# Kernel optimization log

Measured on AMD Instinct MI355X. Metric: run time of the kernel, lower is better.

The kernel has to match this reference:

```python
import jax, jax.numpy as jnp
import numpy as np

B, S, D = 4, 2048, 1024
H = 16
DH = D // H          # 64
DFF = 4096
EPS = 1e-5


def _layer_norm(x, gamma, beta):
    mu = jnp.mean(x, axis=-1, keepdims=True)
    var = jnp.mean(jnp.square(x - mu), axis=-1, keepdims=True)
    return (x - mu) * jax.lax.rsqrt(var + EPS) * gamma + beta


def setup_inputs() -> dict:
    key = jax.random.key(0)
    ks = jax.random.split(key, 8)
    s_in = 1.0 / np.sqrt(D)
    s_ff = 1.0 / np.sqrt(DFF)
    return {
        "x": jax.random.normal(ks[0], (B, S, D), dtype=jnp.float32),
        # per-head qkv weights stacked: [H, D, 3*DH] (nn.Linear, bias=False)
        "Wqkv": jax.random.normal(ks[1], (H, D, 3 * DH), dtype=jnp.float32) * s_in,
        "Wproj": jax.random.normal(ks[2], (D, D), dtype=jnp.float32) * s_in,
        "bproj": jnp.zeros((D,), dtype=jnp.float32),
        "ln1_g": jnp.ones((D,), dtype=jnp.float32),
        "ln1_b": jnp.zeros((D,), dtype=jnp.float32),
        "ln2_g": jnp.ones((D,), dtype=jnp.float32),
        "ln2_b": jnp.zeros((D,), dtype=jnp.float32),
        "W1": jax.random.normal(ks[3], (D, DFF), dtype=jnp.float32) * s_in,
        "b1": jnp.zeros((DFF,), dtype=jnp.float32),
        "W2": jax.random.normal(ks[4], (DFF, D), dtype=jnp.float32) * s_ff,
        "b2": jnp.zeros((D,), dtype=jnp.float32),
    }


def reference(x, Wqkv, Wproj, bproj, ln1_g, ln1_b, ln2_g, ln2_b, W1, b1, W2, b2):
    # fused multi-head QKV projection: [B,S,D] x [H,D,3*DH] -> [B,H,S,3*DH]
    qkv = jnp.einsum('bsd,hde->bhse', x, Wqkv)
    q, k, v = jnp.split(qkv, 3, axis=-1)          # each [B,H,S,DH]
    scale = 1.0 / jnp.sqrt(jnp.asarray(DH, dtype=x.dtype))
    scores = jnp.einsum('bhsd,bhtd->bhst', q, k) * scale   # [B,H,S,S]
    causal = jnp.tril(jnp.ones((S, S), dtype=bool))
    scores = jnp.where(causal, scores, jnp.finfo(x.dtype).min)
    attn = jax.nn.softmax(scores, axis=-1)
    heads = jnp.einsum('bhst,bhtd->bhsd', attn, v)          # [B,H,S,DH]
    att_out = heads.transpose(0, 2, 1, 3).reshape(B, S, D)  # concat heads
    att_out = att_out @ Wproj + bproj
    out = _layer_norm(x + att_out, ln1_g, ln1_b)            # dropout = identity (eval)
    mlp_out = (jax.nn.gelu(out @ W1 + b1, approximate=False)) @ W2 + b2
    out = _layer_norm(out + mlp_out, ln2_g, ln2_b)
    return out
```

## Files before the change

### kernel.cpp

```cpp
#include <hip/hip_runtime.h>
#include <math.h>

#define BB 4
#define SS 2048
#define DD 1024
#define HH 16
#define DHH 64
#define DFF 4096
static constexpr float LN_EPS = 1e-5f;

typedef __bf16 bf16x8 __attribute__((ext_vector_type(8)));
typedef float f32x4 __attribute__((ext_vector_type(4)));
typedef unsigned short u16x8 __attribute__((ext_vector_type(8)));
typedef unsigned int u32x4 __attribute__((ext_vector_type(4)));

__device__ __forceinline__ unsigned short f2bf(float f) {
    return __builtin_bit_cast(unsigned short, (__bf16)f);
}

__device__ __forceinline__ float fexp2(float x) {
    return __builtin_amdgcn_exp2f(x);
}

__device__ __forceinline__ void gl_lds16(const unsigned short* g,
                                         unsigned short* l) {
    __builtin_amdgcn_global_load_lds(
        (const __attribute__((address_space(1))) unsigned int*)g,
        (__attribute__((address_space(3))) unsigned int*)l, 16, 0, 0);
}

#define GBAR()                               \
    do {                                     \
        asm volatile("" ::: "memory");       \
        __builtin_amdgcn_s_barrier();        \
        asm volatile("" ::: "memory");       \
    } while (0)
#define VMCNT(n) asm volatile("s_waitcnt vmcnt(" #n ")" ::: "memory")

__global__ __launch_bounds__(256) void transpose_bf16_kernel(
    const float* __restrict__ in, unsigned short* __restrict__ outT,
    int R, int C) {
    __shared__ float t[64][65];
    const int r0 = blockIdx.y * 64, c0 = blockIdx.x * 64;
    const int cl = threadIdx.x & 63, rl = threadIdx.x >> 6;
#pragma unroll
    for (int rr = 0; rr < 16; ++rr)
        t[rl + rr * 4][cl] = in[(size_t)(r0 + rl + rr * 4) * C + c0 + cl];
    __syncthreads();
#pragma unroll
    for (int rr = 0; rr < 16; ++rr)
        outT[(size_t)(c0 + rl + rr * 4) * R + r0 + cl] = f2bf(t[cl][rl + rr * 4]);
}

__global__ __launch_bounds__(256) void repack_wqkv_bf16_kernel(
    const float* __restrict__ Wqkv, unsigned short* __restrict__ Wq2T) {
    __shared__ float t[64][65];
    const int h = blockIdx.z;
    const int d0 = blockIdx.y * 64, e0 = blockIdx.x * 64;
    const int cl = threadIdx.x & 63, rl = threadIdx.x >> 6;
#pragma unroll
    for (int rr = 0; rr < 16; ++rr)
        t[rl + rr * 4][cl] =
            Wqkv[((size_t)h * DD + d0 + rl + rr * 4) * 192 + e0 + cl];
    __syncthreads();
#pragma unroll
    for (int rr = 0; rr < 16; ++rr)
        Wq2T[((size_t)h * 192 + e0 + rl + rr * 4) * DD + d0 + cl] =
            f2bf(t[cl][rl + rr * 4]);
}

__global__ __launch_bounds__(256) void f2bf_kernel(
    const float* __restrict__ in, unsigned short* __restrict__ out, int n) {
    int i = blockIdx.x * 256 + threadIdx.x;
    if (i < n) out[i] = f2bf(in[i]);
}

template <int RS>
__device__ __forceinline__ void stage_half(const unsigned short* __restrict__ G,
                                           int ldK, int growbase, int kbase,
                                           unsigned short* lbase, int tid) {
#pragma unroll
    for (int s = 0; s < 2; ++s) {
        const int c16 = s * 512 + tid;
        const int r = c16 >> 3, c = c16 & 7;
        const int grow =
            growbase + ((r >> RS) << (RS + 1)) + (r & ((1 << RS) - 1));
        const int gcol = kbase + ((c ^ (r & 7)) << 3);
        gl_lds16(&G[(size_t)grow * ldK + gcol], &lbase[c16 << 3]);
    }
}

__device__ __forceinline__ void stage_64(const unsigned short* __restrict__ G,
                                         int ldK, int growbase, int kbase,
                                         unsigned short* lbase, int tid) {
    const int r = tid >> 3, c = tid & 7;
    const int grow = growbase + ((r >> 5) << 6) + (r & 31);
    const int gcol = kbase + ((c ^ (r & 7)) << 3);
    gl_lds16(&G[(size_t)grow * ldK + gcol], &lbase[tid << 3]);
}

__device__ __forceinline__ void stage_kv(const unsigned short* __restrict__ src,
                                         size_t rstride, unsigned short* dst,
                                         int tid) {
#pragma unroll
    for (int s = 0; s < 2; ++s) {
        const int c16 = s * 256 + tid;
        const int r = c16 >> 3, c = c16 & 7;
        gl_lds16(&src[(size_t)r * rstride + ((c ^ (r & 7)) << 3)],
                 &dst[c16 << 3]);
    }
}

__device__ __forceinline__ void stage_k_pi(const unsigned short* __restrict__ src,
                                           unsigned short* dst, int tid) {
#pragma unroll
    for (int s = 0; s < 2; ++s) {
        const int c16 = s * 256 + tid;
        const int r = c16 >> 3, c = c16 & 7;
        const int gr = ((r >> 4) & 1) * 32 + (((r >> 2) & 3) << 3) +
                       ((r >> 5) & 1) * 4 + (r & 3);
        gl_lds16(&src[(size_t)gr * 64 + ((c ^ (r & 7)) << 3)],
                 &dst[c16 << 3]);
    }
}

__device__ __forceinline__ void read_afrag(const unsigned short* s, int base,
                                           int wm, int l15, int g,
                                           bf16x8 af[4][2]) {
#pragma unroll
    for (int ii = 0; ii < 4; ++ii) {
        const int lr = wm * 64 + ii * 16 + l15;
#pragma unroll
        for (int ks = 0; ks < 2; ++ks) {
            const int p = ((ks << 2) + g) ^ (lr & 7);
            af[ii][ks] = __builtin_bit_cast(
                bf16x8, *(const u16x8*)&s[base + lr * 64 + p * 8]);
        }
    }
}

__device__ __forceinline__ void read_bfrag(const unsigned short* s, int base,
                                           int wn, int l15, int g,
                                           bf16x8 bf2[2][2]) {
#pragma unroll
    for (int jj = 0; jj < 2; ++jj) {
        const int lr = wn * 32 + jj * 16 + l15;
#pragma unroll
        for (int ks = 0; ks < 2; ++ks) {
            const int p = ((ks << 2) + g) ^ (lr & 7);
            bf2[jj][ks] = __builtin_bit_cast(
                bf16x8, *(const u16x8*)&s[base + lr * 64 + p * 8]);
        }
    }
}

template <int MH, int NH>
__device__ __forceinline__ void mfma_quad(f32x4 acc[8][4],
                                          const bf16x8 af[4][2],
                                          const bf16x8 bf2[2][2]) {
    __builtin_amdgcn_s_setprio(1);
#pragma unroll
    for (int ks = 0; ks < 2; ++ks)
#pragma unroll
        for (int ii = 0; ii < 4; ++ii)
#pragma unroll
            for (int jj = 0; jj < 2; ++jj)
                acc[MH * 4 + ii][NH * 2 + jj] =
                    __builtin_amdgcn_mfma_f32_16x16x32_bf16(
                        af[ii][ks], bf2[jj][ks],
                        acc[MH * 4 + ii][NH * 2 + jj], 0, 0, 0);
    __builtin_amdgcn_s_setprio(0);
}

template <int MODE>
__global__ __launch_bounds__(512) void mfma_gemm256_kernel(
    const unsigned short* __restrict__ A, const unsigned short* __restrict__ BT,
    float* __restrict__ Cf, unsigned short* __restrict__ Cb,
    const float* __restrict__ bias, const float* __restrict__ resid,
    int M, int N, int K) {
    __shared__ __align__(16) unsigned short smem[65536];
    const int tid = threadIdx.x;
    const int lane = tid & 63, wave = tid >> 6;
    const int wm = wave >> 2, wn = wave & 3;
    const int l15 = lane & 15, g = lane >> 4;

    const int gx = gridDim.x, nwg = gx * gridDim.y;
    const int lid = blockIdx.y * gx + blockIdx.x;
    const int swz = ((nwg & 7) == 0) ? ((lid & 7) * (nwg >> 3) + (lid >> 3))
                                     : lid;
    const int row0 = (swz / gx) * 256;
    const int col0 = (swz % gx) * 256;

    const int kt = K >> 6;

    f32x4 acc[8][4] = {};

    stage_half<6>(A, K, row0, 0, smem + 0, tid);
    stage_half<6>(A, K, row0 + 64, 0, smem + 8192, tid);
    stage_half<5>(BT, K, col0, 0, smem + 32768, tid);
    stage_half<5>(BT, K, col0 + 32, 0, smem + 40960, tid);
    VMCNT(4);
    stage_half<6>(A, K, row0, 64, smem + 16384, tid);
    stage_half<6>(A, K, row0 + 64, 64, smem + 24576, tid);
    stage_half<5>(BT, K, col0, 64, smem + 49152, tid);
    VMCNT(6);
    GBAR();

    bf16x8 af[4][2], bf0[2][2], bf1[2][2];
    for (int it = 0; it < (kt >> 1); ++it) {
        const int t1k = (2 * it + 1) << 6;
        int t2 = 2 * it + 2; if (t2 > kt - 1) t2 = kt - 1;
        int t3 = 2 * it + 3; if (t3 > kt - 1) t3 = kt - 1;
        const int t2k = t2 << 6, t3k = t3 << 6;

        read_afrag(smem, 0, wm, l15, g, af);
        read_bfrag(smem, 32768, wn, l15, g, bf0);
        stage_half<5>(BT, K, col0 + 32, t1k, smem + 57344, tid);
        GBAR();
        mfma_quad<0, 0>(acc, af, bf0);
        GBAR();

        read_bfrag(smem, 40960, wn, l15, g, bf1);
        stage_half<6>(A, K, row0, t2k, smem + 0, tid);
        GBAR();
        mfma_quad<0, 1>(acc, af, bf1);
        GBAR();

        read_afrag(smem, 8192, wm, l15, g, af);
        stage_half<5>(BT, K, col0, t2k, smem + 32768, tid);
        GBAR();
        mfma_quad<1, 1>(acc, af, bf1);
        GBAR();

        stage_half<6>(A, K, row0 + 64, t2k, smem + 8192, tid);
        GBAR();
        mfma_quad<1, 0>(acc, af, bf0);
        VMCNT(6);
        GBAR();

        read_afrag(smem, 16384, wm, l15, g, af);
        read_bfrag(smem, 49152, wn, l15, g, bf0);
        stage_half<5>(BT, K, col0 + 32, t2k, smem + 40960, tid);
        GBAR();
        mfma_quad<0, 0>(acc, af, bf0);
        GBAR();

        read_bfrag(smem, 57344, wn, l15, g, bf1);
        stage_half<6>(A, K, row0, t3k, smem + 16384, tid);
        GBAR();
        mfma_quad<0, 1>(acc, af, bf1);
        GBAR();

        read_afrag(smem, 24576, wm, l15, g, af);
        stage_half<5>(BT, K, col0, t3k, smem + 49152, tid);
        GBAR();
        mfma_quad<1, 1>(acc, af, bf1);
        GBAR();

        stage_half<6>(A, K, row0 + 64, t3k, smem + 24576, tid);
        GBAR();
        mfma_quad<1, 0>(acc, af, bf0);
        VMCNT(6);
        GBAR();
    }
    VMCNT(0);
    GBAR();

    if (MODE == 2) {
        constexpr int SLAB = 264;
#pragma unroll
        for (int i2 = 0; i2 < 8; ++i2) {
            __syncthreads();
#pragma unroll
            for (int j2 = 0; j2 < 4; ++j2) {
                const int col = wn * 64 + j2 * 16 + l15;
                const float bv = bias[col0 + col];
#pragma unroll
                for (int r = 0; r < 4; ++r) {
                    float v = acc[i2][j2][r] + bv;
                    float t = fexp2(v * (2.30211849f + 0.10294198f * v * v));
                    float gel = v * t * __builtin_amdgcn_rcpf(t + 1.f);
                    smem[(wm * 16 + g * 4 + r) * SLAB + col] = f2bf(gel);
                }
            }
            __syncthreads();
            const int sr = tid >> 4;
            const int cc = (tid & 15) * 16;
            const int grow = row0 + ((sr >> 4) << 7) + i2 * 16 + (sr & 15);
            *(u16x8*)&Cb[(size_t)grow * N + col0 + cc] =
                *(const u16x8*)&smem[sr * SLAB + cc];
            *(u16x8*)&Cb[(size_t)grow * N + col0 + cc + 8] =
                *(const u16x8*)&smem[sr * SLAB + cc + 8];
        }
        return;
    }

#pragma unroll
    for (int i2 = 0; i2 < 8; ++i2) {
#pragma unroll
        for (int j2 = 0; j2 < 4; ++j2) {
            const int col = col0 + wn * 64 + j2 * 16 + l15;
            const int rowb = row0 + wm * 128 + i2 * 16 + g * 4;
            const float bv = bias[col];
#pragma unroll
            for (int r = 0; r < 4; ++r) {
                const int row = rowb + r;
                float v = acc[i2][j2][r] + bv + resid[(size_t)row * N + col];
                Cf[(size_t)row * N + col] = v;
            }
        }
    }
}

__device__ __forceinline__ void read_af128(const unsigned short* s, int base,
                                           int wm, int l15, int g,
                                           bf16x8 af[2][2]) {
#pragma unroll
    for (int ii = 0; ii < 2; ++ii) {
        const int lr = wm * 32 + ii * 16 + l15;
#pragma unroll
        for (int ks = 0; ks < 2; ++ks) {
            const int p = ((ks << 2) + g) ^ (lr & 7);
            af[ii][ks] = __builtin_bit_cast(
                bf16x8, *(const u16x8*)&s[base + lr * 64 + p * 8]);
        }
    }
}

__device__ __forceinline__ void read_bf128(const unsigned short* s, int base,
                                           int wn, int l15, int g,
                                           bf16x8 bf2[2][2]) {
#pragma unroll
    for (int jj = 0; jj < 2; ++jj) {
        const int lr = wn * 32 + jj * 16 + l15;
#pragma unroll
        for (int ks = 0; ks < 2; ++ks) {
            const int p = ((ks << 2) + g) ^ (lr & 7);
            bf2[jj][ks] = __builtin_bit_cast(
                bf16x8, *(const u16x8*)&s[base + lr * 64 + p * 8]);
        }
    }
}

template <int MH, int NH>
__device__ __forceinline__ void mfma_quad128(f32x4 acc[4][4],
                                             const bf16x8 af[2][2],
                                             const bf16x8 bf2[2][2]) {
    __builtin_amdgcn_s_setprio(1);
#pragma unroll
    for (int ks = 0; ks < 2; ++ks)
#pragma unroll
        for (int ii = 0; ii < 2; ++ii)
#pragma unroll
            for (int jj = 0; jj < 2; ++jj)
                acc[MH * 2 + ii][NH * 2 + jj] =
                    __builtin_amdgcn_mfma_f32_16x16x32_bf16(
                        af[ii][ks], bf2[jj][ks],
                        acc[MH * 2 + ii][NH * 2 + jj], 0, 0, 0);
    __builtin_amdgcn_s_setprio(0);
}

template <int MODE>
__global__ __launch_bounds__(512) void gemm_n128_kernel(
    const unsigned short* __restrict__ A, const unsigned short* __restrict__ BT,
    float* __restrict__ Cf, const float* __restrict__ bias,
    const float* __restrict__ resid, unsigned short* __restrict__ Qb,
    unsigned short* __restrict__ Kb, unsigned short* __restrict__ VTb,
    int M, int N, int K) {
    __shared__ __align__(16) unsigned short smem[49152];
    const int tid = threadIdx.x;
    const int lane = tid & 63, wave = tid >> 6;
    const int wm = wave >> 1, wn = wave & 1;
    const int l15 = lane & 15, g = lane >> 4;

    const int gx = gridDim.x, nwg = gx * gridDim.y;
    const int lid = blockIdx.y * gx + blockIdx.x;
    const int swz = ((nwg & 7) == 0) ? ((lid & 7) * (nwg >> 3) + (lid >> 3))
                                     : lid;
    const int row0 = (swz / gx) * 256;
    const int col0 = (swz % gx) * 128;

    const int kt = K >> 6;

    f32x4 acc[4][4] = {};

    stage_half<5>(A, K, row0, 0, smem + 0, tid);
    stage_half<5>(A, K, row0 + 32, 0, smem + 8192, tid);
    stage_64(BT, K, col0, 0, smem + 32768, tid);
    stage_64(BT, K, col0 + 32, 0, smem + 36864, tid);
    VMCNT(4);
    stage_half<5>(A, K, row0, 64, smem + 16384, tid);
    stage_half<5>(A, K, row0 + 32, 64, smem + 24576, tid);
    stage_64(BT, K, col0, 64, smem + 40960, tid);
    VMCNT(5);
    GBAR();

    bf16x8 af[2][2], bf0[2][2], bf1[2][2];
    for (int it = 0; it < (kt >> 1); ++it) {
        const int t1k = (2 * it + 1) << 6;
        int t2 = 2 * it + 2; if (t2 > kt - 1) t2 = kt - 1;
        int t3 = 2 * it + 3; if (t3 > kt - 1) t3 = kt - 1;
        const int t2k = t2 << 6, t3k = t3 << 6;

        read_af128(smem, 0, wm, l15, g, af);
        read_bf128(smem, 32768, wn, l15, g, bf0);
        stage_64(BT, K, col0 + 32, t1k, smem + 45056, tid);
        GBAR();
        mfma_quad128<0, 0>(acc, af, bf0);
        GBAR();

        read_bf128(smem, 36864, wn, l15, g, bf1);
        stage_half<5>(A, K, row0, t2k, smem + 0, tid);
        GBAR();
        mfma_quad128<0, 1>(acc, af, bf1);
        GBAR();

        read_af128(smem, 8192, wm, l15, g, af);
        stage_64(BT, K, col0, t2k, smem + 32768, tid);
        GBAR();
        mfma_quad128<1, 1>(acc, af, bf1);
        GBAR();

        stage_half<5>(A, K, row0 + 32, t2k, smem + 8192, tid);
        GBAR();
        mfma_quad128<1, 0>(acc, af, bf0);
        VMCNT(5);
        GBAR();

        read_af128(smem, 16384, wm, l15, g, af);
        read_bf128(smem, 40960, wn, l15, g, bf0);
        stage_64(BT, K, col0 + 32, t2k, smem + 36864, tid);
        GBAR();
        mfma_quad128<0, 0>(acc, af, bf0);
        GBAR();

        read_bf128(smem, 45056, wn, l15, g, bf1);
        stage_half<5>(A, K, row0, t3k, smem + 16384, tid);
        GBAR();
        mfma_quad128<0, 1>(acc, af, bf1);
        GBAR();

        read_af128(smem, 24576, wm, l15, g, af);
        stage_64(BT, K, col0, t3k, smem + 40960, tid);
        GBAR();
        mfma_quad128<1, 1>(acc, af, bf1);
        GBAR();

        stage_half<5>(A, K, row0 + 32, t3k, smem + 24576, tid);
        GBAR();
        mfma_quad128<1, 0>(acc, af, bf0);
        VMCNT(5);
        GBAR();
    }
    VMCNT(0);
    GBAR();

#pragma unroll
    for (int i2 = 0; i2 < 4; ++i2) {
#pragma unroll
        for (int j2 = 0; j2 < 4; ++j2) {
            const int col = col0 + wn * 64 + j2 * 16 + l15;
            const int rowb = row0 + wm * 64 + i2 * 16 + g * 4;
            if (MODE == 4) {
                const int h = col / 192, e = col % 192;
                const int bb = rowb >> 11, s = rowb & 2047;
                if (e < 64) {
                    unsigned short* q =
                        Qb + (((size_t)bb * HH + h) * SS + s) * 64 + e;
#pragma unroll
                    for (int r = 0; r < 4; ++r)
                        q[r * 64] = f2bf(acc[i2][j2][r] * 0.18033688f);
                } else if (e < 128) {
                    unsigned short* kp =
                        Kb + (((size_t)bb * HH + h) * SS + s) * 64 + (e - 64);
#pragma unroll
                    for (int r = 0; r < 4; ++r)
                        kp[r * 64] = f2bf(acc[i2][j2][r]);
                } else {
                    ushort4 pk;
                    pk.x = f2bf(acc[i2][j2][0]);
                    pk.y = f2bf(acc[i2][j2][1]);
                    pk.z = f2bf(acc[i2][j2][2]);
                    pk.w = f2bf(acc[i2][j2][3]);
                    *(ushort4*)(VTb + (((size_t)bb * HH + h) * 64 + (e - 128)) *
                                          SS + s) = pk;
                }
            } else {
                const float bv = bias[col];
#pragma unroll
                for (int r = 0; r < 4; ++r) {
                    const int row = rowb + r;
                    float v = acc[i2][j2][r] + bv + resid[(size_t)row * N + col];
                    Cf[(size_t)row * N + col] = v;
                }
            }
        }
    }
}

__global__ __launch_bounds__(256, 2) void fattn_kernel(
    const unsigned short* __restrict__ Qb, const unsigned short* __restrict__ Kb,
    const unsigned short* __restrict__ VTb, unsigned short* __restrict__ att) {
    __shared__ __align__(16) unsigned short Kls[2][64 * 64];
    __shared__ __align__(16) unsigned short VTls[2][64 * 64];

    const int bh = blockIdx.x;
    const int p = blockIdx.y;
    const int tid = threadIdx.x;
    const int lane = tid & 63;
    const int wave = tid >> 6;
    const int l15 = lane & 15;
    const int g = lane >> 4;
    const int b = bh >> 4, h = bh & 15;
    const int xh = l15 & 7;

    const unsigned short* Qh = Qb + (size_t)bh * SS * 64;
    const unsigned short* Kh = Kb + (size_t)bh * SS * 64;
    const unsigned short* Vh = VTb + (size_t)bh * 64 * SS;

#pragma unroll 1
    for (int half = 0; half < 2; ++half) {
        const int cidx = half ? (15 - p) : p;
        const int q0c = cidx << 7;
        const int qw = q0c + wave * 32;
        const int qlim = qw + 31;
        const int nt = (cidx << 1) + 2;

        bf16x8 qf[2][2];
#pragma unroll
        for (int i = 0; i < 2; ++i)
#pragma unroll
            for (int ks = 0; ks < 2; ++ks)
                qf[i][ks] = __builtin_bit_cast(
                    bf16x8, *(const u16x8*)&Qh[(size_t)(qw + i * 16 + l15) * 64 +
                                               ks * 32 + g * 8]);

        f32x4 oacc[4][2] = {};
        float mst[2], lst[2];
#pragma unroll
        for (int i = 0; i < 2; ++i) { mst[i] = -1e30f; lst[i] = 0.f; }

        stage_k_pi(Kh, &Kls[0][0], tid);
        stage_kv(Vh, SS, &VTls[0][0], tid);

        for (int t = 0; t < nt; ++t) {
            const int t0 = t << 6;
            if (t + 1 < nt) {
                stage_k_pi(Kh + ((size_t)(t + 1) << 6) * 64,
                           &Kls[(t + 1) & 1][0], tid);
                stage_kv(Vh + ((t + 1) << 6), SS, &VTls[(t + 1) & 1][0], tid);
                VMCNT(4);
            } else {
                VMCNT(0);
            }
            GBAR();

            if (t0 <= qlim) {
                const unsigned short* Kt = &Kls[t & 1][0];
                const unsigned short* Vt = &VTls[t & 1][0];

                f32x4 sacc[4][2] = {};
                __builtin_amdgcn_s_setprio(1);
#pragma unroll
                for (int ks = 0; ks < 2; ++ks) {
                    const int ko = ((((ks << 2) + g) ^ xh) << 3);
                    bf16x8 kb[4];
#pragma unroll
                    for (int j = 0; j < 4; ++j)
                        kb[j] = __builtin_bit_cast(
                            bf16x8,
                            *(const u16x8*)&Kt[(j * 16 + l15) * 64 + ko]);
#pragma unroll
                    for (int j = 0; j < 4; ++j)
#pragma unroll
                        for (int i = 0; i < 2; ++i)
                            sacc[j][i] =
                                __builtin_amdgcn_mfma_f32_16x16x32_bf16(
                                    kb[j], qf[i][ks], sacc[j][i], 0, 0, 0);
                }
                __builtin_amdgcn_s_setprio(0);

                if (t0 + 63 > qw) {
#pragma unroll
                    for (int j = 0; j < 4; ++j) {
                        const int kgb = t0 + ((j & 1) << 5) + (g << 3) +
                                        ((j >> 1) << 2);
#pragma unroll
                        for (int i = 0; i < 2; ++i) {
                            const int qgi = qw + i * 16 + l15;
#pragma unroll
                            for (int r = 0; r < 4; ++r)
                                if (kgb + r > qgi) sacc[j][i][r] = -1e30f;
                        }
                    }
                }

                unsigned int Aw[2][4], Bw[2][4];
#pragma unroll
                for (int i = 0; i < 2; ++i) {
                    float mx = -1e30f;
#pragma unroll
                    for (int j = 0; j < 4; ++j)
                        mx = fmaxf(mx,
                                   fmaxf(fmaxf(sacc[j][i][0], sacc[j][i][1]),
                                         fmaxf(sacc[j][i][2], sacc[j][i][3])));
                    mx = fmaxf(mx, __shfl_xor(mx, 16));
                    mx = fmaxf(mx, __shfl_xor(mx, 32));
                    const bool grow = !__all(mx <= mst[i]);
                    float al = 1.f;
                    if (grow) {
                        const float mn = fmaxf(mst[i], mx);
                        al = fexp2(mst[i] - mn);
                        mst[i] = mn;
                    }
                    const float mm = mst[i];
                    float rsum = 0.f;
#pragma unroll
                    for (int j = 0; j < 4; ++j) {
                        float p0 = fexp2(sacc[j][i][0] - mm);
                        float p1 = fexp2(sacc[j][i][1] - mm);
                        float p2 = fexp2(sacc[j][i][2] - mm);
                        float p3 = fexp2(sacc[j][i][3] - mm);
                        rsum += (p0 + p1) + (p2 + p3);
                        Aw[i][j] = (unsigned int)f2bf(p0) |
                                   ((unsigned int)f2bf(p1) << 16);
                        Bw[i][j] = (unsigned int)f2bf(p2) |
                                   ((unsigned int)f2bf(p3) << 16);
                    }
                    rsum += __shfl_xor(rsum, 16);
                    rsum += __shfl_xor(rsum, 32);
                    if (grow) {
                        lst[i] = lst[i] * al + rsum;
#pragma unroll
                        for (int jo = 0; jo < 4; ++jo)
#pragma unroll
                            for (int r = 0; r < 4; ++r) oacc[jo][i][r] *= al;
                    } else {
                        lst[i] += rsum;
                    }
                }

#pragma unroll
                for (int ks = 0; ks < 2; ++ks) {
                    const int ko = ((((ks << 2) + g) ^ xh) << 3);
                    bf16x8 vb[4];
#pragma unroll
                    for (int jo = 0; jo < 4; ++jo)
                        vb[jo] = __builtin_bit_cast(
                            bf16x8,
                            *(const u16x8*)&Vt[(jo * 16 + l15) * 64 + ko]);
                    __builtin_amdgcn_s_setprio(1);
#pragma unroll
                    for (int i = 0; i < 2; ++i) {
                        u32x4 pw;
                        pw[0] = Aw[i][ks];
                        pw[1] = Bw[i][ks];
                        pw[2] = Aw[i][2 + ks];
                        pw[3] = Bw[i][2 + ks];
                        const bf16x8 pf = __builtin_bit_cast(bf16x8, pw);
#pragma unroll
                        for (int jo = 0; jo < 4; ++jo)
                            oacc[jo][i] =
                                __builtin_amdgcn_mfma_f32_16x16x32_bf16(
                                    vb[jo], pf, oacc[jo][i], 0, 0, 0);
                    }
                    __builtin_amdgcn_s_setprio(0);
                }
            }
            GBAR();
        }

#pragma unroll
        for (int i = 0; i < 2; ++i) {
            const float inv = 1.f / lst[i];
            const int qg = qw + i * 16 + l15;
            unsigned short* dst =
                att + ((size_t)b * SS + qg) * DD + h * 64 + g * 4;
#pragma unroll
            for (int jo = 0; jo < 4; ++jo) {
                ushort4 pk;
                pk.x = f2bf(oacc[jo][i][0] * inv);
                pk.y = f2bf(oacc[jo][i][1] * inv);
                pk.z = f2bf(oacc[jo][i][2] * inv);
                pk.w = f2bf(oacc[jo][i][3] * inv);
                *(ushort4*)(dst + jo * 16) = pk;
            }
        }
        GBAR();
    }
}

__global__ __launch_bounds__(256) void ln_kernel(
    const float* __restrict__ X, const float* __restrict__ g,
    const float* __restrict__ bta, float* __restrict__ Y,
    unsigned short* __restrict__ Yb) {
    const int row = blockIdx.x;
    const float4 xv = ((const float4*)(X + (size_t)row * DD))[threadIdx.x];

    __shared__ float red1[4], red2[4];
    float s = xv.x + xv.y + xv.z + xv.w;
#pragma unroll
    for (int off = 32; off > 0; off >>= 1) s += __shfl_down(s, off);
    const int wave = threadIdx.x >> 6;
    if ((threadIdx.x & 63) == 0) red1[wave] = s;
    __syncthreads();
    const float mu = (red1[0] + red1[1] + red1[2] + red1[3]) * (1.f / DD);

    float dx = xv.x - mu, dy = xv.y - mu, dz = xv.z - mu, dw = xv.w - mu;
    float s2 = dx * dx + dy * dy + dz * dz + dw * dw;
#pragma unroll
    for (int off = 32; off > 0; off >>= 1) s2 += __shfl_down(s2, off);
    if ((threadIdx.x & 63) == 0) red2[wave] = s2;
    __syncthreads();
    const float var = (red2[0] + red2[1] + red2[2] + red2[3]) * (1.f / DD);
    const float rstd = rsqrtf(var + LN_EPS);

    const float4 gv = ((const float4*)g)[threadIdx.x];
    const float4 bv = ((const float4*)bta)[threadIdx.x];
    float4 yv;
    yv.x = dx * rstd * gv.x + bv.x;
    yv.y = dy * rstd * gv.y + bv.y;
    yv.z = dz * rstd * gv.z + bv.z;
    yv.w = dw * rstd * gv.w + bv.w;
    ((float4*)(Y + (size_t)row * DD))[threadIdx.x] = yv;
    if (Yb) {
        ushort4 q;
        q.x = f2bf(yv.x); q.y = f2bf(yv.y);
        q.z = f2bf(yv.z); q.w = f2bf(yv.w);
        ((ushort4*)(Yb + (size_t)row * DD))[threadIdx.x] = q;
    }
}

extern "C" void kernel_launch(void* const* d_in, const int* in_sizes, int n_in,
                              void* d_out, int out_size, void* d_ws,
                              size_t ws_size, hipStream_t stream) {
    const float* x     = (const float*)d_in[0];
    const float* Wqkv  = (const float*)d_in[1];
    const float* Wproj = (const float*)d_in[2];
    const float* bproj = (const float*)d_in[3];
    const float* ln1_g = (const float*)d_in[4];
    const float* ln1_b = (const float*)d_in[5];
    const float* ln2_g = (const float*)d_in[6];
    const float* ln2_b = (const float*)d_in[7];
    const float* W1    = (const float*)d_in[8];
    const float* b1    = (const float*)d_in[9];
    const float* W2    = (const float*)d_in[10];
    const float* b2    = (const float*)d_in[11];
    float* out = (float*)d_out;

    const size_t M = (size_t)BB * SS;
    const size_t MB = 1024 * 1024;
    char* w = (char*)d_ws;
    unsigned short* Qb     = (unsigned short*)(w + 0);
    unsigned short* out1b  = (unsigned short*)(w + 0);
    unsigned short* Kb     = (unsigned short*)(w + 16 * MB);
    unsigned short* VTb    = (unsigned short*)(w + 32 * MB);
    unsigned short* hbuf   = (unsigned short*)(w + 16 * MB);
    unsigned short* Wq2T   = (unsigned short*)(w + 96 * MB);
    unsigned short* xb     = (unsigned short*)(w + 102 * MB);
    unsigned short* att    = (unsigned short*)(w + 96 * MB);
    float*          out1   = (float*)(w + 96 * MB);
    unsigned short* WprojT = (unsigned short*)(w + 118 * MB);
    unsigned short* W1T    = (unsigned short*)(w + 128 * MB);
    unsigned short* W2T    = (unsigned short*)(w + 136 * MB);

    repack_wqkv_bf16_kernel<<<dim3(3, 16, 16), 256, 0, stream>>>(Wqkv, Wq2T);
    transpose_bf16_kernel<<<dim3(16, 16), 256, 0, stream>>>(Wproj, WprojT, 1024, 1024);
    transpose_bf16_kernel<<<dim3(64, 16), 256, 0, stream>>>(W1, W1T, 1024, 4096);
    transpose_bf16_kernel<<<dim3(16, 64), 256, 0, stream>>>(W2, W2T, 4096, 1024);
    f2bf_kernel<<<(int)((M * DD + 255) / 256), 256, 0, stream>>>(x, xb, (int)(M * DD));

    gemm_n128_kernel<4><<<dim3(3072 / 128, M / 256), 512, 0, stream>>>(
        xb, Wq2T, nullptr, nullptr, nullptr, Qb, Kb, VTb, (int)M, 3072, 1024);

    fattn_kernel<<<dim3(BB * HH, 8), 256, 0, stream>>>(Qb, Kb, VTb, att);

    gemm_n128_kernel<3><<<dim3(1024 / 128, M / 256), 512, 0, stream>>>(
        att, WprojT, out, bproj, x, nullptr, nullptr, nullptr,
        (int)M, 1024, 1024);

    ln_kernel<<<(int)M, 256, 0, stream>>>(out, ln1_g, ln1_b, out1, out1b);

    mfma_gemm256_kernel<2><<<dim3(4096 / 256, M / 256), 512, 0, stream>>>(
        out1b, W1T, nullptr, hbuf, b1, nullptr, (int)M, 4096, 1024);

    gemm_n128_kernel<3><<<dim3(1024 / 128, M / 256), 512, 0, stream>>>(
        hbuf, W2T, out, b2, out1, nullptr, nullptr, nullptr,
        (int)M, 1024, 4096);

    ln_kernel<<<(int)M, 256, 0, stream>>>(out, ln2_g, ln2_b, out, nullptr);
}
```

Before: 477.5 us.

## Shrink n128 GEMM tile to 128x128 with 256 threads and 2 blocks/CU

Converts the 256x128-tile, 512-thread GEMM used for QKV, projection and W2 into a 128x128-tile, 256-thread kernel with half the shared memory and launch bounds allowing two blocks per CU. The staging helper now loads 64-row halves in two passes, the LDS buffer offsets and vmcnt waits are reworked, and the grid doubles in the M dimension. This aims to improve occupancy and wave-count balance across CUs, especially for the N=1024 GEMMs, at the cost of less data reuse per tile and more global traffic.

```diff
diff --git a/kernel.cpp b/kernel.cpp
--- a/kernel.cpp
+++ b/kernel.cpp
@@ -90,13 +90,17 @@
     }
 }
 
-__device__ __forceinline__ void stage_64(const unsigned short* __restrict__ G,
-                                         int ldK, int growbase, int kbase,
-                                         unsigned short* lbase, int tid) {
-    const int r = tid >> 3, c = tid & 7;
-    const int grow = growbase + ((r >> 5) << 6) + (r & 31);
-    const int gcol = kbase + ((c ^ (r & 7)) << 3);
-    gl_lds16(&G[(size_t)grow * ldK + gcol], &lbase[tid << 3]);
+__device__ __forceinline__ void stage_h64(const unsigned short* __restrict__ G,
+                                          int ldK, int growbase, int kbase,
+                                          unsigned short* lbase, int tid) {
+#pragma unroll
+    for (int s = 0; s < 2; ++s) {
+        const int c16 = s * 256 + tid;
+        const int r = c16 >> 3, c = c16 & 7;
+        const int grow = growbase + ((r >> 5) << 6) + (r & 31);
+        const int gcol = kbase + ((c ^ (r & 7)) << 3);
+        gl_lds16(&G[(size_t)grow * ldK + gcol], &lbase[c16 << 3]);
+    }
 }
 
 __device__ __forceinline__ void stage_kv(const unsigned short* __restrict__ src,
@@ -361,13 +365,13 @@
 }
 
 template <int MODE>
-__global__ __launch_bounds__(512) void gemm_n128_kernel(
+__global__ __launch_bounds__(256, 2) void gemm128_kernel(
     const unsigned short* __restrict__ A, const unsigned short* __restrict__ BT,
     float* __restrict__ Cf, const float* __restrict__ bias,
     const float* __restrict__ resid, unsigned short* __restrict__ Qb,
     unsigned short* __restrict__ Kb, unsigned short* __restrict__ VTb,
     int M, int N, int K) {
-    __shared__ __align__(16) unsigned short smem[49152];
+    __shared__ __align__(16) unsigned short smem[32768];
     const int tid = threadIdx.x;
     const int lane = tid & 63, wave = tid >> 6;
     const int wm = wave >> 1, wn = wave & 1;
@@ -377,22 +381,22 @@
     const int lid = blockIdx.y * gx + blockIdx.x;
     const int swz = ((nwg & 7) == 0) ? ((lid & 7) * (nwg >> 3) + (lid >> 3))
                                      : lid;
-    const int row0 = (swz / gx) * 256;
+    const int row0 = (swz / gx) * 128;
     const int col0 = (swz % gx) * 128;
 
     const int kt = K >> 6;
 
     f32x4 acc[4][4] = {};
 
-    stage_half<5>(A, K, row0, 0, smem + 0, tid);
-    stage_half<5>(A, K, row0 + 32, 0, smem + 8192, tid);
-    stage_64(BT, K, col0, 0, smem + 32768, tid);
-    stage_64(BT, K, col0 + 32, 0, smem + 36864, tid);
+    stage_h64(A, K, row0, 0, smem + 0, tid);
+    stage_h64(A, K, row0 + 32, 0, smem + 4096, tid);
+    stage_h64(BT, K, col0, 0, smem + 16384, tid);
+    stage_h64(BT, K, col0 + 32, 0, smem + 20480, tid);
     VMCNT(4);
-    stage_half<5>(A, K, row0, 64, smem + 16384, tid);
-    stage_half<5>(A, K, row0 + 32, 64, smem + 24576, tid);
-    stage_64(BT, K, col0, 64, smem + 40960, tid);
-    VMCNT(5);
+    stage_h64(A, K, row0, 64, smem + 8192, tid);
+    stage_h64(A, K, row0 + 32, 64, smem + 12288, tid);
+    stage_h64(BT, K, col0, 64, smem + 24576, tid);
+    VMCNT(6);
     GBAR();
 
     bf16x8 af[2][2], bf0[2][2], bf1[2][2];
@@ -403,53 +407,53 @@
         const int t2k = t2 << 6, t3k = t3 << 6;
 
         read_af128(smem, 0, wm, l15, g, af);
-        read_bf128(smem, 32768, wn, l15, g, bf0);
-        stage_64(BT, K, col0 + 32, t1k, smem + 45056, tid);
+        read_bf128(smem, 16384, wn, l15, g, bf0);
+        stage_h64(BT, K, col0 + 32, t1k, smem + 28672, tid);
         GBAR();
         mfma_quad128<0, 0>(acc, af, bf0);
         GBAR();
 
-        read_bf128(smem, 36864, wn, l15, g, bf1);
-        stage_half<5>(A, K, row0, t2k, smem + 0, tid);
+        read_bf128(smem, 20480, wn, l15, g, bf1);
+        stage_h64(A, K, row0, t2k, smem + 0, tid);
         GBAR();
         mfma_quad128<0, 1>(acc, af, bf1);
         GBAR();
 
+        read_af128(smem, 4096, wm, l15, g, af);
+        stage_h64(BT, K, col0, t2k, smem + 16384, tid);
+        GBAR();
+        mfma_quad128<1, 1>(acc, af, bf1);
+        GBAR();
+
+        stage_h64(A, K, row0 + 32, t2k, smem + 4096, tid);
+        GBAR();
+        mfma_quad128<1, 0>(acc, af, bf0);
+        VMCNT(6);
+        GBAR();
+
         read_af128(smem, 8192, wm, l15, g, af);
-        stage_64(BT, K, col0, t2k, smem + 32768, tid);
+        read_bf128(smem, 24576, wn, l15, g, bf0);
+        stage_h64(BT, K, col0 + 32, t2k, smem + 20480, tid);
+        GBAR();
+        mfma_quad128<0, 0>(acc, af, bf0);
+        GBAR();
+
+        read_bf128(smem, 28672, wn, l15, g, bf1);
+        stage_h64(A, K, row0, t3k, smem + 8192, tid);
+        GBAR();
+        mfma_quad128<0, 1>(acc, af, bf1);
+        GBAR();
+
+        read_af128(smem, 12288, wm, l15, g, af);
+        stage_h64(BT, K, col0, t3k, smem + 24576, tid);
         GBAR();
         mfma_quad128<1, 1>(acc, af, bf1);
         GBAR();
 
-        stage_half<5>(A, K, row0 + 32, t2k, smem + 8192, tid);
+        stage_h64(A, K, row0 + 32, t3k, smem + 12288, tid);
         GBAR();
         mfma_quad128<1, 0>(acc, af, bf0);
-        VMCNT(5);
-        GBAR();
-
-        read_af128(smem, 16384, wm, l15, g, af);
-        read_bf128(smem, 40960, wn, l15, g, bf0);
-        stage_64(BT, K, col0 + 32, t2k, smem + 36864, tid);
-        GBAR();
-        mfma_quad128<0, 0>(acc, af, bf0);
-        GBAR();
-
-        read_bf128(smem, 45056, wn, l15, g, bf1);
-        stage_half<5>(A, K, row0, t3k, smem + 16384, tid);
-        GBAR();
-        mfma_quad128<0, 1>(acc, af, bf1);
-        GBAR();
-
-        read_af128(smem, 24576, wm, l15, g, af);
-        stage_64(BT, K, col0, t3k, smem + 40960, tid);
-        GBAR();
-        mfma_quad128<1, 1>(acc, af, bf1);
-        GBAR();
-
-        stage_half<5>(A, K, row0 + 32, t3k, smem + 24576, tid);
-        GBAR();
-        mfma_quad128<1, 0>(acc, af, bf0);
-        VMCNT(5);
+        VMCNT(6);
         GBAR();
     }
     VMCNT(0);
@@ -770,12 +774,12 @@
     transpose_bf16_kernel<<<dim3(16, 64), 256, 0, stream>>>(W2, W2T, 4096, 1024);
     f2bf_kernel<<<(int)((M * DD + 255) / 256), 256, 0, stream>>>(x, xb, (int)(M * DD));
 
-    gemm_n128_kernel<4><<<dim3(3072 / 128, M / 256), 512, 0, stream>>>(
+    gemm128_kernel<4><<<dim3(3072 / 128, M / 128), 256, 0, stream>>>(
         xb, Wq2T, nullptr, nullptr, nullptr, Qb, Kb, VTb, (int)M, 3072, 1024);
 
     fattn_kernel<<<dim3(BB * HH, 8), 256, 0, stream>>>(Qb, Kb, VTb, att);
 
-    gemm_n128_kernel<3><<<dim3(1024 / 128, M / 256), 512, 0, stream>>>(
+    gemm128_kernel<3><<<dim3(1024 / 128, M / 128), 256, 0, stream>>>(
         att, WprojT, out, bproj, x, nullptr, nullptr, nullptr,
         (int)M, 1024, 1024);
 
@@ -784,7 +788,7 @@
     mfma_gemm256_kernel<2><<<dim3(4096 / 256, M / 256), 512, 0, stream>>>(
         out1b, W1T, nullptr, hbuf, b1, nullptr, (int)M, 4096, 1024);
 
-    gemm_n128_kernel<3><<<dim3(1024 / 128, M / 256), 512, 0, stream>>>(
+    gemm128_kernel<3><<<dim3(1024 / 128, M / 128), 256, 0, stream>>>(
         hbuf, W2T, out, b2, out1, nullptr, nullptr, nullptr,
         (int)M, 1024, 4096);
 
```

After: 477.8 us. Within noise of the previous version (+0.1%).
